# Kernel optimization log

Hardware: AMD Instinct MI355X
Metric: run time of the kernel (lower is better)

The kernel has to match this reference:

```python
import jax, jax.numpy as jnp
import numpy as np


def setup_inputs() -> dict:
    key = jax.random.key(0)
    ip = jax.random.normal(key, (8, 256, 128, 128), dtype=jnp.float32)
    return {"ip": ip}


def reference(ip):
    b, C, H, W = ip.shape
    two_c = 2 * C
    # precomputed complex shift grid: exp(-1j*2*pi*(C-0.5)*v/(2C)), v = 0..2C-1
    v = jnp.arange(two_c, dtype=jnp.float32)
    angle = -2.0 * jnp.pi * (C - 0.5) * v / two_c
    shift = (jnp.cos(angle) + 1j * jnp.sin(angle)).astype(jnp.complex64)  # [2C]

    viDct = ip * two_c                                   # [b, C, H, W]
    flip_neg = -viDct[:, 1:][:, ::-1]                    # [b, C-1, H, W]
    zeros = jnp.zeros((b, 1, H, W), dtype=ip.dtype)
    rev = jnp.concatenate([viDct, zeros, flip_neg], axis=1)  # [b, 2C, H, W]
    rev = rev.astype(jnp.complex64) * shift[None, :, None, None]
    vxx = jnp.fft.ifft(rev, axis=1)                      # norm='backward' (default)
    out = vxx[:, :C][:, ::-1].real                       # first C, flipped, real part
    return out.astype(ip.dtype)
```

## Files before the change

### kernel.cpp

```cpp
#include <hip/hip_runtime.h>
#include <math.h>

#define NB   8
#define NC   256
#define NHW  (128 * 128)

#define TILES 4
#define XB 65536

typedef __attribute__((ext_vector_type(4))) float f32x4;
typedef __attribute__((ext_vector_type(8))) short bf16x8;
typedef __attribute__((ext_vector_type(4))) unsigned int u32x4;

__device__ __forceinline__ unsigned short f2bf(float f) {
    unsigned u = __builtin_bit_cast(unsigned, f);
    u += 0x7fffu + ((u >> 16) & 1u);
    return (unsigned short)(u >> 16);
}

__device__ __forceinline__ unsigned pack2bf(float a, float b) {
    unsigned lo = __builtin_bit_cast(unsigned, a);
    lo += 0x7fffu + ((lo >> 16) & 1u);
    unsigned hi = __builtin_bit_cast(unsigned, b);
    hi += 0x7fffu + ((hi >> 16) & 1u);
    return (lo >> 16) | (hi & 0xffff0000u);
}

__device__ __forceinline__ bf16x8 flip_odd(bf16x8 b) {
    u32x4 u = __builtin_bit_cast(u32x4, b);
    u ^= (u32x4){0x80000000u, 0x80000000u, 0x80000000u, 0x80000000u};
    return __builtin_bit_cast(bf16x8, u);
}

__global__ void coef_kernel(unsigned short* __restrict__ coef) {
    int idx = blockIdx.x * 256 + threadIdx.x;
    int c = idx >> 8;
    int k = idx & 255;
    int t = (k * (2 * c + 1)) & 1023;
    float v = (k == 0) ? 1.0f : 2.0f * cosf((float)t * (float)(M_PI / 512.0));
    coef[idx] = f2bf(v);
}

__device__ __forceinline__ void gload_lds16(const void* g, void* l) {
    __builtin_amdgcn_global_load_lds(
        (const __attribute__((address_space(1))) unsigned int*)g,
        (__attribute__((address_space(3))) unsigned int*)l,
        16, 0, 0);
}


__global__ __launch_bounds__(512, 2)
void dct_gemm(const float* __restrict__ X, const unsigned short* __restrict__ Mcoef,
              float* __restrict__ Out) {
    __shared__ __align__(16) unsigned char lds[131072];

    const int tid  = threadIdx.x;
    const int lane = tid & 63;
    const int wave = tid >> 6;
    const int m16  = lane & 15;
    const int quad = lane >> 4;
    const int wm   = wave >> 1;
    const int wn   = wave & 1;

#pragma unroll
    for (int i = 0; i < 8; i++) {
        const int L = i * 8192 + tid * 16;
        const int row = L >> 9;
        const int sl = ((L >> 4) & 31) ^ (row & 15);
        gload_lds16(Mcoef + row * 256 + sl * 8, lds + L);
    }

    const int sp  = tid & 63;
    const int skb = wave * 32;

    const int g0 = blockIdx.x * TILES;

    {
        const float* s = X + (size_t)(g0 >> 8) * (NC * NHW) + (size_t)skb * NHW + (g0 & 255) * 64 + sp;
        float v[32];
#pragma unroll
        for (int j = 0; j < 32; j++) v[j] = s[(size_t)j * NHW];
#pragma unroll
        for (int w = 0; w < 4; w++) {
            int4 q = { (int)pack2bf(v[8*w+0], v[8*w+1]), (int)pack2bf(v[8*w+2], v[8*w+3]),
                       (int)pack2bf(v[8*w+4], v[8*w+5]), (int)pack2bf(v[8*w+6], v[8*w+7]) };
            *(int4*)(lds + XB + sp * 512 + (((wave * 4 + w) ^ (sp & 15)) << 4)) = q;
        }
    }
    __syncthreads();

    const int aB0 = (wm * 32 + m16) * 512;
    const int xB0 = (wn * 32 + m16) * 512;

    for (int t = 0; t < TILES; t++) {
        const int g = g0 + t;
        const unsigned char* Xc = lds + XB + (t & 1) * 32768;
        unsigned char* Xs = lds + XB + ((t + 1) & 1) * 32768;

        float v[32];
        if (t + 1 < TILES) {
            const int g1 = g + 1;
            const float* s = X + (size_t)(g1 >> 8) * (NC * NHW) + (size_t)skb * NHW + (g1 & 255) * 64 + sp;
#pragma unroll
            for (int j = 0; j < 32; j++) v[j] = s[(size_t)j * NHW];
        }

        f32x4 acc[2][2][2];
#pragma unroll
        for (int a = 0; a < 2; a++)
#pragma unroll
            for (int b = 0; b < 2; b++)
#pragma unroll
                for (int h = 0; h < 2; h++) acc[a][b][h] = (f32x4){0.f, 0.f, 0.f, 0.f};

#pragma unroll
        for (int kk = 0; kk < 8; kk++) {
            const int so = (((kk * 4 + quad) ^ m16) << 4);
            bf16x8 af0 = *(const bf16x8*)(lds + aB0 + so);
            bf16x8 af1 = *(const bf16x8*)(lds + aB0 + 16 * 512 + so);
            bf16x8 bf0 = *(const bf16x8*)(Xc + xB0 + so);
            bf16x8 bf1 = *(const bf16x8*)(Xc + xB0 + 16 * 512 + so);
            bf16x8 bn0 = flip_odd(bf0);
            bf16x8 bn1 = flip_odd(bf1);
            acc[0][0][0] = __builtin_amdgcn_mfma_f32_16x16x32_bf16(af0, bf0, acc[0][0][0], 0, 0, 0);
            acc[0][1][0] = __builtin_amdgcn_mfma_f32_16x16x32_bf16(af0, bf1, acc[0][1][0], 0, 0, 0);
            acc[1][0][0] = __builtin_amdgcn_mfma_f32_16x16x32_bf16(af1, bf0, acc[1][0][0], 0, 0, 0);
            acc[1][1][0] = __builtin_amdgcn_mfma_f32_16x16x32_bf16(af1, bf1, acc[1][1][0], 0, 0, 0);
            acc[0][0][1] = __builtin_amdgcn_mfma_f32_16x16x32_bf16(af0, bn0, acc[0][0][1], 0, 0, 0);
            acc[0][1][1] = __builtin_amdgcn_mfma_f32_16x16x32_bf16(af0, bn1, acc[0][1][1], 0, 0, 0);
            acc[1][0][1] = __builtin_amdgcn_mfma_f32_16x16x32_bf16(af1, bn0, acc[1][0][1], 0, 0, 0);
            acc[1][1][1] = __builtin_amdgcn_mfma_f32_16x16x32_bf16(af1, bn1, acc[1][1][1], 0, 0, 0);
        }

        if (t + 1 < TILES) {
#pragma unroll
            for (int w = 0; w < 4; w++) {
                int4 q = { (int)pack2bf(v[8*w+0], v[8*w+1]), (int)pack2bf(v[8*w+2], v[8*w+3]),
                           (int)pack2bf(v[8*w+4], v[8*w+5]), (int)pack2bf(v[8*w+6], v[8*w+7]) };
                *(int4*)(Xs + sp * 512 + (((wave * 4 + w) ^ (sp & 15)) << 4)) = q;
            }
        }

        float* Ob = Out + (size_t)(g >> 8) * (NC * NHW) + (g & 255) * 64;
#pragma unroll
        for (int mt = 0; mt < 2; mt++) {
            const int cL = wm * 32 + mt * 16 + quad * 4;
#pragma unroll
            for (int nt = 0; nt < 2; nt++) {
                const int pp = wn * 32 + nt * 16 + m16;
#pragma unroll
                for (int r = 0; r < 4; r++) {
                    Ob[(size_t)(cL + r) * NHW + pp]       = acc[mt][nt][0][r];
                    Ob[(size_t)(255 - cL - r) * NHW + pp] = acc[mt][nt][1][r];
                }
            }
        }

        if (t + 1 < TILES) __syncthreads();
    }
}

extern "C" void kernel_launch(void* const* d_in, const int* in_sizes, int n_in,
                              void* d_out, int out_size, void* d_ws, size_t ws_size,
                              hipStream_t stream) {
    const float* ip = (const float*)d_in[0];
    float* out = (float*)d_out;
    unsigned short* coef = (unsigned short*)d_ws;

    coef_kernel<<<dim3(128), dim3(256), 0, stream>>>(coef);

    dct_gemm<<<dim3(512), dim3(512), 0, stream>>>(ip, coef, out);
}
```

Measured before the change: 243.9 us.

## Drop LDS staging; load coefficients and inputs directly from global into MFMA fragments

Removes the shared-memory staging of the coefficient matrix and the double-buffered input tiles. Each wave now reads its A fragments straight from global (cached) and its B values as strided fp32 loads packed to bf16 in registers. Each block covers 32 pixels with 256 threads over a 2D grid, and the multi-tile loop is gone. This drops the LDS traffic and barriers and raises occupancy. In exchange, every block re-reads the full coefficient matrix from cache, and the 32-wide fp32 loads are only half-coalesced.

```diff
diff --git a/kernel.cpp b/kernel.cpp
--- a/kernel.cpp
+++ b/kernel.cpp
@@ -5,8 +5,6 @@
 #define NC   256
 #define NHW  (128 * 128)
 
-#define TILES 4
-#define XB 65536
 
 typedef __attribute__((ext_vector_type(4))) float f32x4;
 typedef __attribute__((ext_vector_type(8))) short bf16x8;
@@ -41,122 +39,80 @@
     coef[idx] = f2bf(v);
 }
 
-__device__ __forceinline__ void gload_lds16(const void* g, void* l) {
-    __builtin_amdgcn_global_load_lds(
-        (const __attribute__((address_space(1))) unsigned int*)g,
-        (__attribute__((address_space(3))) unsigned int*)l,
-        16, 0, 0);
-}
-
-
-__global__ __launch_bounds__(512, 2)
+__global__ __launch_bounds__(256, 4)
 void dct_gemm(const float* __restrict__ X, const unsigned short* __restrict__ Mcoef,
               float* __restrict__ Out) {
-    __shared__ __align__(16) unsigned char lds[131072];
-
     const int tid  = threadIdx.x;
     const int lane = tid & 63;
     const int wave = tid >> 6;
     const int m16  = lane & 15;
     const int quad = lane >> 4;
-    const int wm   = wave >> 1;
-    const int wn   = wave & 1;
+
+    const int p0 = blockIdx.x * 32;
+    const size_t base = (size_t)blockIdx.y * (NC * NHW);
+    const float* Xb = X + base + p0;
+    float* Ob = Out + base + p0;
+
+    const unsigned short* aP0 = Mcoef + (wave * 32 + m16) * NC + quad * 8;
+    const unsigned short* aP1 = aP0 + 16 * NC;
+
+    const float* bP = Xb + (size_t)(quad * 8) * NHW + m16;
+
+    f32x4 acc[2][2][2];
+#pragma unroll
+    for (int a = 0; a < 2; a++)
+#pragma unroll
+        for (int b = 0; b < 2; b++)
+#pragma unroll
+            for (int h = 0; h < 2; h++) acc[a][b][h] = (f32x4){0.f, 0.f, 0.f, 0.f};
 
 #pragma unroll
-    for (int i = 0; i < 8; i++) {
-        const int L = i * 8192 + tid * 16;
-        const int row = L >> 9;
-        const int sl = ((L >> 4) & 31) ^ (row & 15);
-        gload_lds16(Mcoef + row * 256 + sl * 8, lds + L);
+    for (int kk = 0; kk < 8; kk++) {
+        const int kb = kk * 32;
+
+        bf16x8 af0 = *(const bf16x8*)(aP0 + kb);
+        bf16x8 af1 = *(const bf16x8*)(aP1 + kb);
+
+        float fb[2][8];
+#pragma unroll
+        for (int nt = 0; nt < 2; nt++)
+#pragma unroll
+            for (int j = 0; j < 8; j++)
+                fb[nt][j] = bP[(size_t)(kb + j) * NHW + nt * 16];
+
+        bf16x8 bf[2], bn[2];
+#pragma unroll
+        for (int nt = 0; nt < 2; nt++) {
+            u32x4 pk;
+#pragma unroll
+            for (int j = 0; j < 4; j++)
+                pk[j] = pack2bf(fb[nt][2 * j], fb[nt][2 * j + 1]);
+            bf[nt] = __builtin_bit_cast(bf16x8, pk);
+            bn[nt] = flip_odd(bf[nt]);
+        }
+
+        acc[0][0][0] = __builtin_amdgcn_mfma_f32_16x16x32_bf16(af0, bf[0], acc[0][0][0], 0, 0, 0);
+        acc[0][1][0] = __builtin_amdgcn_mfma_f32_16x16x32_bf16(af0, bf[1], acc[0][1][0], 0, 0, 0);
+        acc[1][0][0] = __builtin_amdgcn_mfma_f32_16x16x32_bf16(af1, bf[0], acc[1][0][0], 0, 0, 0);
+        acc[1][1][0] = __builtin_amdgcn_mfma_f32_16x16x32_bf16(af1, bf[1], acc[1][1][0], 0, 0, 0);
+        acc[0][0][1] = __builtin_amdgcn_mfma_f32_16x16x32_bf16(af0, bn[0], acc[0][0][1], 0, 0, 0);
+        acc[0][1][1] = __builtin_amdgcn_mfma_f32_16x16x32_bf16(af0, bn[1], acc[0][1][1], 0, 0, 0);
+        acc[1][0][1] = __builtin_amdgcn_mfma_f32_16x16x32_bf16(af1, bn[0], acc[1][0][1], 0, 0, 0);
+        acc[1][1][1] = __builtin_amdgcn_mfma_f32_16x16x32_bf16(af1, bn[1], acc[1][1][1], 0, 0, 0);
     }
 
-    const int sp  = tid & 63;
-    const int skb = wave * 32;
-
-    const int g0 = blockIdx.x * TILES;
-
-    {
-        const float* s = X + (size_t)(g0 >> 8) * (NC * NHW) + (size_t)skb * NHW + (g0 & 255) * 64 + sp;
-        float v[32];
 #pragma unroll
-        for (int j = 0; j < 32; j++) v[j] = s[(size_t)j * NHW];
+    for (int mt = 0; mt < 2; mt++) {
+        const int cS = wave * 32 + mt * 16 + quad * 4;
 #pragma unroll
-        for (int w = 0; w < 4; w++) {
-            int4 q = { (int)pack2bf(v[8*w+0], v[8*w+1]), (int)pack2bf(v[8*w+2], v[8*w+3]),
-                       (int)pack2bf(v[8*w+4], v[8*w+5]), (int)pack2bf(v[8*w+6], v[8*w+7]) };
-            *(int4*)(lds + XB + sp * 512 + (((wave * 4 + w) ^ (sp & 15)) << 4)) = q;
-        }
-    }
-    __syncthreads();
-
-    const int aB0 = (wm * 32 + m16) * 512;
-    const int xB0 = (wn * 32 + m16) * 512;
-
-    for (int t = 0; t < TILES; t++) {
-        const int g = g0 + t;
-        const unsigned char* Xc = lds + XB + (t & 1) * 32768;
-        unsigned char* Xs = lds + XB + ((t + 1) & 1) * 32768;
-
-        float v[32];
-        if (t + 1 < TILES) {
-            const int g1 = g + 1;
-            const float* s = X + (size_t)(g1 >> 8) * (NC * NHW) + (size_t)skb * NHW + (g1 & 255) * 64 + sp;
+        for (int nt = 0; nt < 2; nt++) {
+            float* o = Ob + nt * 16 + m16;
 #pragma unroll
-            for (int j = 0; j < 32; j++) v[j] = s[(size_t)j * NHW];
-        }
-
-        f32x4 acc[2][2][2];
-#pragma unroll
-        for (int a = 0; a < 2; a++)
-#pragma unroll
-            for (int b = 0; b < 2; b++)
-#pragma unroll
-                for (int h = 0; h < 2; h++) acc[a][b][h] = (f32x4){0.f, 0.f, 0.f, 0.f};
-
-#pragma unroll
-        for (int kk = 0; kk < 8; kk++) {
-            const int so = (((kk * 4 + quad) ^ m16) << 4);
-            bf16x8 af0 = *(const bf16x8*)(lds + aB0 + so);
-            bf16x8 af1 = *(const bf16x8*)(lds + aB0 + 16 * 512 + so);
-            bf16x8 bf0 = *(const bf16x8*)(Xc + xB0 + so);
-            bf16x8 bf1 = *(const bf16x8*)(Xc + xB0 + 16 * 512 + so);
-            bf16x8 bn0 = flip_odd(bf0);
-            bf16x8 bn1 = flip_odd(bf1);
-            acc[0][0][0] = __builtin_amdgcn_mfma_f32_16x16x32_bf16(af0, bf0, acc[0][0][0], 0, 0, 0);
-            acc[0][1][0] = __builtin_amdgcn_mfma_f32_16x16x32_bf16(af0, bf1, acc[0][1][0], 0, 0, 0);
-            acc[1][0][0] = __builtin_amdgcn_mfma_f32_16x16x32_bf16(af1, bf0, acc[1][0][0], 0, 0, 0);
-            acc[1][1][0] = __builtin_amdgcn_mfma_f32_16x16x32_bf16(af1, bf1, acc[1][1][0], 0, 0, 0);
-            acc[0][0][1] = __builtin_amdgcn_mfma_f32_16x16x32_bf16(af0, bn0, acc[0][0][1], 0, 0, 0);
-            acc[0][1][1] = __builtin_amdgcn_mfma_f32_16x16x32_bf16(af0, bn1, acc[0][1][1], 0, 0, 0);
-            acc[1][0][1] = __builtin_amdgcn_mfma_f32_16x16x32_bf16(af1, bn0, acc[1][0][1], 0, 0, 0);
-            acc[1][1][1] = __builtin_amdgcn_mfma_f32_16x16x32_bf16(af1, bn1, acc[1][1][1], 0, 0, 0);
-        }
-
-        if (t + 1 < TILES) {
-#pragma unroll
-            for (int w = 0; w < 4; w++) {
-                int4 q = { (int)pack2bf(v[8*w+0], v[8*w+1]), (int)pack2bf(v[8*w+2], v[8*w+3]),
-                           (int)pack2bf(v[8*w+4], v[8*w+5]), (int)pack2bf(v[8*w+6], v[8*w+7]) };
-                *(int4*)(Xs + sp * 512 + (((wave * 4 + w) ^ (sp & 15)) << 4)) = q;
+            for (int r = 0; r < 4; r++) {
+                o[(size_t)(cS + r) * NHW]       = acc[mt][nt][0][r];
+                o[(size_t)(255 - cS - r) * NHW] = acc[mt][nt][1][r];
             }
         }
-
-        float* Ob = Out + (size_t)(g >> 8) * (NC * NHW) + (g & 255) * 64;
-#pragma unroll
-        for (int mt = 0; mt < 2; mt++) {
-            const int cL = wm * 32 + mt * 16 + quad * 4;
-#pragma unroll
-            for (int nt = 0; nt < 2; nt++) {
-                const int pp = wn * 32 + nt * 16 + m16;
-#pragma unroll
-                for (int r = 0; r < 4; r++) {
-                    Ob[(size_t)(cL + r) * NHW + pp]       = acc[mt][nt][0][r];
-                    Ob[(size_t)(255 - cL - r) * NHW + pp] = acc[mt][nt][1][r];
-                }
-            }
-        }
-
-        if (t + 1 < TILES) __syncthreads();
     }
 }
 
@@ -169,5 +125,5 @@
 
     coef_kernel<<<dim3(128), dim3(256), 0, stream>>>(coef);
 
-    dct_gemm<<<dim3(512), dim3(512), 0, stream>>>(ip, coef, out);
+    dct_gemm<<<dim3(NHW / 32, NB), dim3(256), 0, stream>>>(ip, coef, out);
 }
```

Result: slower. 292.2 us (+19.8%).
